# Kernel optimization log

Hardware: AMD Instinct MI355X
Metric: run time of the kernel (lower is better)

The kernel has to match this reference:

```python
import jax, jax.numpy as jnp
import numpy as np

B, N, CIN, COUT = 2, 4096, 128, 64

def setup_inputs() -> dict:
    key = jax.random.key(0)
    ks = jax.random.split(key, 9)
    s1 = 1.0 / np.sqrt(CIN)
    s2 = 1.0 / np.sqrt(COUT)
    sa = 1.0 / np.sqrt(2 * COUT)
    return {
        "x": jax.random.normal(ks[0], (B, N, CIN), dtype=jnp.float32),
        "adj_matrix": jax.random.uniform(ks[1], (B, N, N), dtype=jnp.float32),
        "W1": jax.random.uniform(ks[2], (CIN, COUT), jnp.float32, -s1, s1),
        "b1": jax.random.uniform(ks[3], (COUT,), jnp.float32, -s1, s1),
        "W2": jax.random.uniform(ks[4], (COUT, COUT), jnp.float32, -s2, s2),
        "b2": jax.random.uniform(ks[5], (COUT,), jnp.float32, -s2, s2),
        "Wa": jax.random.uniform(ks[6], (2 * COUT, 1), jnp.float32, -sa, sa),
        "ba": jax.random.uniform(ks[7], (1,), jnp.float32, -sa, sa),
    }

def reference(x, adj_matrix, W1, b1, W2, b2, Wa, ba):
    # conv: two Linear+ReLU layers -> h [B,N,C]
    h = jax.nn.relu(jnp.einsum('bni,io->bno', x, W1) + b1)
    h = jax.nn.relu(jnp.einsum('bni,io->bno', h, W2) + b2)
    # attention Linear(2C,1) on cat[h_i, h_j] factorizes: e_ij = sigmoid(u_i + v_j + b)
    C = h.shape[-1]
    u = jnp.einsum('bnc,c->bn', h, Wa[:C, 0])  # contribution of node i (row)
    v = jnp.einsum('bnc,c->bn', h, Wa[C:, 0])  # contribution of node j (col)
    e = jax.nn.sigmoid(u[:, :, None] + v[:, None, :] + ba[0])  # [B,N,N]
    a = e * adj_matrix
    a = a / (jnp.sum(a, axis=-1, keepdims=True) + 1e-10)
    h_out = jnp.einsum('bnm,bmc->bnc', a, h)
    return (h_out, a)
```

## Files before the change

### kernel.cpp

```cpp
#include <hip/hip_runtime.h>

#define BB 2
#define NN 4096
#define CIN 128
#define CC 64
#define JT 256
#define NTILES (NN / JT)

typedef __attribute__((ext_vector_type(4))) float floatx4;
typedef __attribute__((ext_vector_type(8))) short short8;
typedef __attribute__((ext_vector_type(4))) short short4v;

__device__ __forceinline__ short f2bf(float f) {
    unsigned u = __float_as_uint(f);
    u += 0x7fffu + ((u >> 16) & 1u);
    return (short)(u >> 16);
}

__device__ __forceinline__ float sigf(float x) {
    return __builtin_amdgcn_rcpf(1.0f + __expf(-x));
}

__device__ __forceinline__ void lbar() {
    asm volatile("s_waitcnt lgkmcnt(0)" ::: "memory");
    __builtin_amdgcn_s_barrier();
}

__global__ __launch_bounds__(256) void feat_v3(
    const float* __restrict__ x, const float* __restrict__ W1,
    const float* __restrict__ b1, const float* __restrict__ W2,
    const float* __restrict__ b2, const float* __restrict__ Wa,
    const float* __restrict__ ba,
    short* __restrict__ hT, float* __restrict__ u, float* __restrict__ v)
{
    __shared__ float W1s[CIN * CC];
    __shared__ float W2s[CC * CC];
    __shared__ float xs[16 * 132];
    __shared__ float h1s[16 * 68];
    __shared__ __align__(16) short hs[CC][16];

    const int t = threadIdx.x;
    const int row0 = blockIdx.x * 16;

    {
        const floatx4* s1 = (const floatx4*)W1;
        floatx4* d1 = (floatx4*)W1s;
        for (int i = t; i < CIN * CC / 4; i += 256) d1[i] = s1[i];
        const floatx4* s2 = (const floatx4*)W2;
        floatx4* d2 = (floatx4*)W2s;
        for (int i = t; i < CC * CC / 4; i += 256) d2[i] = s2[i];
        const floatx4* sx = (const floatx4*)(x + (size_t)row0 * CIN);
        for (int i = t; i < 16 * CIN / 4; i += 256) {
            int rw = i >> 5, c4 = i & 31;
            *(floatx4*)(xs + rw * 132 + c4 * 4) = sx[i];
        }
    }
    __syncthreads();

    const int n  = t >> 4;
    const int cg = t & 15;
    const int c0 = cg * 4;

    float acc[4];
#pragma unroll
    for (int i = 0; i < 4; i++) acc[i] = b1[c0 + i];
    for (int k = 0; k < CIN; k++) {
        float a = xs[n * 132 + k];
        const floatx4 w = *(const floatx4*)&W1s[k * CC + c0];
#pragma unroll
        for (int i = 0; i < 4; i++) acc[i] = fmaf(a, w[i], acc[i]);
    }
#pragma unroll
    for (int i = 0; i < 4; i++) h1s[n * 68 + c0 + i] = fmaxf(acc[i], 0.0f);
    __syncthreads();

    float acc2[4];
#pragma unroll
    for (int i = 0; i < 4; i++) acc2[i] = b2[c0 + i];
    for (int k = 0; k < CC; k++) {
        float a = h1s[n * 68 + k];
        const floatx4 w = *(const floatx4*)&W2s[k * CC + c0];
#pragma unroll
        for (int i = 0; i < 4; i++) acc2[i] = fmaf(a, w[i], acc2[i]);
    }
#pragma unroll
    for (int i = 0; i < 4; i++) acc2[i] = fmaxf(acc2[i], 0.0f);

#pragma unroll
    for (int i = 0; i < 4; i++) hs[c0 + i][n] = f2bf(acc2[i]);

    float pu = 0.0f, pv = 0.0f;
#pragma unroll
    for (int i = 0; i < 4; i++) {
        pu = fmaf(acc2[i], Wa[c0 + i], pu);
        pv = fmaf(acc2[i], Wa[CC + c0 + i], pv);
    }
    pu += __shfl_down(pu, 8, 16); pv += __shfl_down(pv, 8, 16);
    pu += __shfl_down(pu, 4, 16); pv += __shfl_down(pv, 4, 16);
    pu += __shfl_down(pu, 2, 16); pv += __shfl_down(pv, 2, 16);
    pu += __shfl_down(pu, 1, 16); pv += __shfl_down(pv, 1, 16);

    const int grow = row0 + n;
    if (cg == 0) { u[grow] = pu + ba[0]; v[grow] = pv; }

    __syncthreads();
    if (t < 128) {
        const int c  = t >> 1;
        const int hf = t & 1;
        const int b   = row0 >> 12;
        const int nn0 = row0 & (NN - 1);
        *(short8*)(hT + ((size_t)(b * CC + c)) * NN + nn0 + hf * 8) =
            *(const short8*)&hs[c][hf * 8];
    }
}

__global__ __launch_bounds__(512, 4) void attn_v4(
    const float* __restrict__ adj, const float* __restrict__ u,
    const float* __restrict__ v, const short* __restrict__ hT,
    float* __restrict__ hout, float* __restrict__ aout)
{
    __shared__ __align__(16) short P[2][16][264];
    __shared__ float red[4][16][17];

    const int wave = threadIdx.x >> 6;
    const int lane = threadIdx.x & 63;
    const int quad = lane >> 4;
    const int m16  = lane & 15;

    const int row0 = blockIdx.x * 16;
    const int b  = row0 >> 12;
    const int n0 = row0 & (NN - 1);
    const float* vb = v + b * NN;

    const int r0 = 2 * wave;
    const float u0 = u[b * NN + n0 + r0];
    const float u1 = u[b * NN + n0 + r0 + 1];
    const float* a0p = adj + ((size_t)(b * NN + n0 + r0)) * NN;
    const float* a1p = a0p + NN;
    float* o0p = aout + ((size_t)(b * NN + n0 + r0)) * NN;
    float* o1p = o0p + NN;

    float s0 = 0.f, s1 = 0.f;
#pragma unroll 4
    for (int c = 0; c < 16; ++c) {
        const int j = c * 256 + lane * 4;
        const floatx4 va = *(const floatx4*)(vb + j);
        const floatx4 aa = *(const floatx4*)(a0p + j);
        const floatx4 ab = *(const floatx4*)(a1p + j);
#pragma unroll
        for (int i = 0; i < 4; ++i) {
            s0 = fmaf(aa[i], sigf(u0 + va[i]), s0);
            s1 = fmaf(ab[i], sigf(u1 + va[i]), s1);
        }
    }
#pragma unroll
    for (int off = 32; off; off >>= 1) {
        s0 += __shfl_down(s0, off);
        s1 += __shfl_down(s1, off);
    }
    s0 = __shfl(s0, 0);
    s1 = __shfl(s1, 0);
    const float ir0 = __builtin_amdgcn_rcpf(s0 + 1e-10f);
    const float ir1 = __builtin_amdgcn_rcpf(s1 + 1e-10f);

    const int c0 = (wave & 3) * 16;
    const int kh = wave >> 2;
    const short* hp = hT + ((size_t)(b * CC + c0 + m16)) * NN;

    floatx4 acc = (floatx4){0.f, 0.f, 0.f, 0.f};

#define FILL(T, BUF) { \
    const int j = (T) * JT + lane * 4; \
    const floatx4 va = *(const floatx4*)(vb + j); \
    const floatx4 aa = *(const floatx4*)(a0p + j); \
    const floatx4 ab = *(const floatx4*)(a1p + j); \
    floatx4 o0, o1; short4v pk0, pk1; \
    _Pragma("unroll") \
    for (int i = 0; i < 4; ++i) { \
        float sA = aa[i] * sigf(u0 + va[i]) * ir0; \
        float sB = ab[i] * sigf(u1 + va[i]) * ir1; \
        o0[i] = sA; o1[i] = sB; \
        pk0[i] = f2bf(sA); pk1[i] = f2bf(sB); } \
    __builtin_nontemporal_store(o0, (floatx4*)(o0p + j)); \
    __builtin_nontemporal_store(o1, (floatx4*)(o1p + j)); \
    *(short4v*)&P[BUF][r0][lane * 4]     = pk0; \
    *(short4v*)&P[BUF][r0 + 1][lane * 4] = pk1; }

#define MM(T, BUF) { \
    const short* hpt = hp + (size_t)(T) * JT; \
    _Pragma("unroll") \
    for (int ks = 0; ks < 4; ++ks) { \
        const int kk = kh * 4 + ks; \
        const short8 Af = *(const short8*)&P[BUF][m16][kk * 32 + quad * 8]; \
        const short8 Bf = *(const short8*)(hpt + kk * 32 + quad * 8); \
        acc = __builtin_amdgcn_mfma_f32_16x16x32_bf16(Af, Bf, acc, 0, 0, 0); \
    } }

    FILL(0, 0)
    lbar();
#pragma unroll 2
    for (int t = 0; t < NTILES; ++t) {
        if (t + 1 < NTILES) { FILL(t + 1, (t + 1) & 1) }
        MM(t, t & 1)
        lbar();
    }
#undef FILL
#undef MM

    if (kh == 1) {
#pragma unroll
        for (int i = 0; i < 4; ++i) red[wave - 4][quad * 4 + i][m16] = acc[i];
    }
    __syncthreads();
    if (kh == 0) {
#pragma unroll
        for (int i = 0; i < 4; ++i) {
            const float sfin = acc[i] + red[wave][quad * 4 + i][m16];
            hout[((size_t)(b * NN + n0 + quad * 4 + i)) * CC + c0 + m16] = sfin;
        }
    }
}

extern "C" void kernel_launch(void* const* d_in, const int* in_sizes, int n_in,
                              void* d_out, int out_size, void* d_ws, size_t ws_size,
                              hipStream_t stream) {
    (void)in_sizes; (void)n_in; (void)out_size; (void)ws_size;
    const float* x   = (const float*)d_in[0];
    const float* adj = (const float*)d_in[1];
    const float* W1  = (const float*)d_in[2];
    const float* b1  = (const float*)d_in[3];
    const float* W2  = (const float*)d_in[4];
    const float* b2  = (const float*)d_in[5];
    const float* Wa  = (const float*)d_in[6];
    const float* ba  = (const float*)d_in[7];

    float* hout = (float*)d_out;
    float* aout = hout + (size_t)BB * NN * CC;

    char* ws = (char*)d_ws;
    short* hT = (short*)ws;
    float* u  = (float*)(ws + (size_t)BB * CC * NN * sizeof(short));
    float* vv = u + BB * NN;

    feat_v3<<<BB * NN / 16, 256, 0, stream>>>(x, W1, b1, W2, b2, Wa, ba, hT, u, vv);
    attn_v4<<<BB * NN / 16, 512, 0, stream>>>(adj, u, vv, hT, hout, aout);
}
```

Before: 289.7 us.

## Restructure attention kernel with register-prefetched loads and two large LDS phases

The row-sum pass now keeps two groups of adj/v loads in flight, double-buffered in registers, with 8 floats per lane instead of 4. The main pass replaces the 16-tile double-buffered LDS loop with two half-row phases: each phase fills a 2048-wide bf16 P buffer and then runs 32 MFMAs per wave. This cuts the barrier count from 16 to 3 and overlaps global loads with compute. In exchange it uses more registers and a larger LDS buffer (about 66KB), which may reduce occupancy below the 4 blocks per CU the launch bounds request.

```diff
diff --git a/kernel.cpp b/kernel.cpp
--- a/kernel.cpp
+++ b/kernel.cpp
@@ -4,12 +4,9 @@
 #define NN 4096
 #define CIN 128
 #define CC 64
-#define JT 256
-#define NTILES (NN / JT)
 
 typedef __attribute__((ext_vector_type(4))) float floatx4;
 typedef __attribute__((ext_vector_type(8))) short short8;
-typedef __attribute__((ext_vector_type(4))) short short4v;
 
 __device__ __forceinline__ short f2bf(float f) {
     unsigned u = __float_as_uint(f);
@@ -114,12 +111,12 @@
     }
 }
 
-__global__ __launch_bounds__(512, 4) void attn_v4(
+__global__ __launch_bounds__(512, 4) void attn_v5(
     const float* __restrict__ adj, const float* __restrict__ u,
     const float* __restrict__ v, const short* __restrict__ hT,
     float* __restrict__ hout, float* __restrict__ aout)
 {
-    __shared__ __align__(16) short P[2][16][264];
+    __shared__ __align__(16) short P[16][2056];
     __shared__ float red[4][16][17];
 
     const int wave = threadIdx.x >> 6;
@@ -140,19 +137,32 @@
     float* o0p = aout + ((size_t)(b * NN + n0 + r0)) * NN;
     float* o1p = o0p + NN;
 
+    floatx4 vA0, vA1, aA0, aA1, bA0, bA1;
+    floatx4 vB0, vB1, aB0, aB1, bB0, bB1;
+
+#define LDA(S, J) { const int j_ = (J) + lane * 8; \
+    v##S##0 = *(const floatx4*)(vb  + j_); v##S##1 = *(const floatx4*)(vb  + j_ + 4); \
+    a##S##0 = *(const floatx4*)(a0p + j_); a##S##1 = *(const floatx4*)(a0p + j_ + 4); \
+    b##S##0 = *(const floatx4*)(a1p + j_); b##S##1 = *(const floatx4*)(a1p + j_ + 4); }
+
+#define SUMA(S) { \
+    _Pragma("unroll") \
+    for (int i = 0; i < 4; ++i) { \
+        s0 = fmaf(a##S##0[i], sigf(u0 + v##S##0[i]), s0); \
+        s0 = fmaf(a##S##1[i], sigf(u0 + v##S##1[i]), s0); \
+        s1 = fmaf(b##S##0[i], sigf(u1 + v##S##0[i]), s1); \
+        s1 = fmaf(b##S##1[i], sigf(u1 + v##S##1[i]), s1); } }
+
     float s0 = 0.f, s1 = 0.f;
-#pragma unroll 4
-    for (int c = 0; c < 16; ++c) {
-        const int j = c * 256 + lane * 4;
-        const floatx4 va = *(const floatx4*)(vb + j);
-        const floatx4 aa = *(const floatx4*)(a0p + j);
-        const floatx4 ab = *(const floatx4*)(a1p + j);
-#pragma unroll
-        for (int i = 0; i < 4; ++i) {
-            s0 = fmaf(aa[i], sigf(u0 + va[i]), s0);
-            s1 = fmaf(ab[i], sigf(u1 + va[i]), s1);
-        }
-    }
+    LDA(A, 0)    LDA(B, 512)
+    SUMA(A)      LDA(A, 1024)
+    SUMA(B)      LDA(B, 1536)
+    SUMA(A)      LDA(A, 2048)
+    SUMA(B)      LDA(B, 2560)
+    SUMA(A)      LDA(A, 3072)
+    SUMA(B)      LDA(B, 3584)
+    SUMA(A)      SUMA(B)
+
 #pragma unroll
     for (int off = 32; off; off >>= 1) {
         s0 += __shfl_down(s0, off);
@@ -163,60 +173,70 @@
     const float ir0 = __builtin_amdgcn_rcpf(s0 + 1e-10f);
     const float ir1 = __builtin_amdgcn_rcpf(s1 + 1e-10f);
 
-    const int c0 = (wave & 3) * 16;
+    const int cg = wave & 3;
     const int kh = wave >> 2;
-    const short* hp = hT + ((size_t)(b * CC + c0 + m16)) * NN;
+    const short* hpbase = hT + ((size_t)(b * CC + cg * 16 + m16)) * NN + kh * 1024;
 
     floatx4 acc = (floatx4){0.f, 0.f, 0.f, 0.f};
 
-#define FILL(T, BUF) { \
-    const int j = (T) * JT + lane * 4; \
-    const floatx4 va = *(const floatx4*)(vb + j); \
-    const floatx4 aa = *(const floatx4*)(a0p + j); \
-    const floatx4 ab = *(const floatx4*)(a1p + j); \
-    floatx4 o0, o1; short4v pk0, pk1; \
+#define PB(S, JG, JL) { \
+    const int j_  = (JG) + lane * 8; \
+    const int jl_ = (JL) + lane * 8; \
+    floatx4 o00, o01, o10, o11; short8 p0, p1; \
     _Pragma("unroll") \
     for (int i = 0; i < 4; ++i) { \
-        float sA = aa[i] * sigf(u0 + va[i]) * ir0; \
-        float sB = ab[i] * sigf(u1 + va[i]) * ir1; \
-        o0[i] = sA; o1[i] = sB; \
-        pk0[i] = f2bf(sA); pk1[i] = f2bf(sB); } \
-    __builtin_nontemporal_store(o0, (floatx4*)(o0p + j)); \
-    __builtin_nontemporal_store(o1, (floatx4*)(o1p + j)); \
-    *(short4v*)&P[BUF][r0][lane * 4]     = pk0; \
-    *(short4v*)&P[BUF][r0 + 1][lane * 4] = pk1; }
-
-#define MM(T, BUF) { \
-    const short* hpt = hp + (size_t)(T) * JT; \
-    _Pragma("unroll") \
-    for (int ks = 0; ks < 4; ++ks) { \
-        const int kk = kh * 4 + ks; \
-        const short8 Af = *(const short8*)&P[BUF][m16][kk * 32 + quad * 8]; \
-        const short8 Bf = *(const short8*)(hpt + kk * 32 + quad * 8); \
-        acc = __builtin_amdgcn_mfma_f32_16x16x32_bf16(Af, Bf, acc, 0, 0, 0); \
-    } }
-
-    FILL(0, 0)
+        float x0 = a##S##0[i] * sigf(u0 + v##S##0[i]) * ir0; \
+        float x1 = a##S##1[i] * sigf(u0 + v##S##1[i]) * ir0; \
+        float y0 = b##S##0[i] * sigf(u1 + v##S##0[i]) * ir1; \
+        float y1 = b##S##1[i] * sigf(u1 + v##S##1[i]) * ir1; \
+        o00[i] = x0; o01[i] = x1; o10[i] = y0; o11[i] = y1; \
+        p0[i] = f2bf(x0); p0[4 + i] = f2bf(x1); \
+        p1[i] = f2bf(y0); p1[4 + i] = f2bf(y1); } \
+    __builtin_nontemporal_store(o00, (floatx4*)(o0p + j_)); \
+    __builtin_nontemporal_store(o01, (floatx4*)(o0p + j_ + 4)); \
+    __builtin_nontemporal_store(o10, (floatx4*)(o1p + j_)); \
+    __builtin_nontemporal_store(o11, (floatx4*)(o1p + j_ + 4)); \
+    *(short8*)&P[r0][jl_]     = p0; \
+    *(short8*)&P[r0 + 1][jl_] = p1; }
+
+#define MMH(JB) { \
+    const short* hq = hpbase + (JB); \
+    _Pragma("unroll 8") \
+    for (int s2 = 0; s2 < 32; ++s2) { \
+        const short8 Af = *(const short8*)&P[m16][kh * 1024 + s2 * 32 + quad * 8]; \
+        const short8 Bf = *(const short8*)(hq + s2 * 32 + quad * 8); \
+        acc = __builtin_amdgcn_mfma_f32_16x16x32_bf16(Af, Bf, acc, 0, 0, 0); } }
+
+    LDA(A, 0)           LDA(B, 512)
+    PB(A, 0, 0)         LDA(A, 1024)
+    PB(B, 512, 512)     LDA(B, 1536)
+    PB(A, 1024, 1024)   PB(B, 1536, 1536)
+    LDA(A, 2048)        LDA(B, 2560)
     lbar();
-#pragma unroll 2
-    for (int t = 0; t < NTILES; ++t) {
-        if (t + 1 < NTILES) { FILL(t + 1, (t + 1) & 1) }
-        MM(t, t & 1)
-        lbar();
-    }
-#undef FILL
-#undef MM
+    MMH(0)
+    lbar();
+
+    PB(A, 2048, 0)      LDA(A, 3072)
+    PB(B, 2560, 512)    LDA(B, 3584)
+    PB(A, 3072, 1024)   PB(B, 3584, 1536)
+    lbar();
+    MMH(2048)
+
+#undef LDA
+#undef SUMA
+#undef PB
+#undef MMH
 
     if (kh == 1) {
 #pragma unroll
-        for (int i = 0; i < 4; ++i) red[wave - 4][quad * 4 + i][m16] = acc[i];
+        for (int i = 0; i < 4; ++i) red[cg][quad * 4 + i][m16] = acc[i];
     }
     __syncthreads();
     if (kh == 0) {
 #pragma unroll
         for (int i = 0; i < 4; ++i) {
-            const float sfin = acc[i] + red[wave][quad * 4 + i][m16];
-            hout[((size_t)(b * NN + n0 + quad * 4 + i)) * CC + c0 + m16] = sfin;
+            const float sfin = acc[i] + red[cg][quad * 4 + i][m16];
+            hout[((size_t)(b * NN + n0 + quad * 4 + i)) * CC + cg * 16 + m16] = sfin;
         }
     }
 }
@@ -243,5 +263,5 @@
     float* vv = u + BB * NN;
 
     feat_v3<<<BB * NN / 16, 256, 0, stream>>>(x, W1, b1, W2, b2, Wa, ba, hT, u, vv);
-    attn_v4<<<BB * NN / 16, 512, 0, stream>>>(adj, u, vv, hT, hout, aout);
-}
+    attn_v5<<<BB * NN / 16, 512, 0, stream>>>(adj, u, vv, hT, hout, aout);
+}
```

Result: slower. 379.3 us (+30.9%).
